# Kernel optimization log

Measured on AMD Instinct MI355X. Metric: run time of the kernel, lower is better.

Reference implementation:

```python
import jax, jax.numpy as jnp
import numpy as np

ALPHA = 0.2  # LeakyReLU negative slope


def setup_inputs() -> dict:
    key = jax.random.key(0)
    k0, k1, k2, k3 = jax.random.split(key, 4)
    N, H, W, T, V = 16, 32, 32, 16, 64
    h = jax.random.normal(k0, (N, H, W, T, V), jnp.float32)
    conv_w = jax.random.normal(k1, (3, 3, T, T), jnp.float32) * 0.05  # HWIO
    conv_b = jnp.zeros((T,), jnp.float32)
    a = jax.random.normal(k2, (2 * H * W, 1), jnp.float32) * 0.03  # ~xavier scale
    B = jax.random.uniform(k3, (V, V), jnp.float32)
    return {"h": h, "conv_w": conv_w, "conv_b": conv_b, "a": a, "B": B}


def reference(h, conv_w, conv_b, a, B):
    N, H, W, T, V = h.shape
    hv = jnp.transpose(h, (0, 4, 1, 2, 3))  # (N,V,H,W,T)

    # ConvMapping: 3x3 SAME conv over spatial dims with T as channels
    x = hv.reshape(N * V, H, W, T)
    y = jax.lax.conv_general_dilated(
        x, conv_w, (1, 1), 'SAME',
        dimension_numbers=('NHWC', 'HWIO', 'NHWC')) + conv_b
    Wh = y.reshape(N, V, H, W, T)

    # Attention logits. Original builds concat([Wh_i, Wh_j], dim=W) with trailing
    # layout (H, 2W, T) then row-major views it as (T, 2*H*W). We reproduce that
    # exact reinterpretation, but exploit additivity over i/j so the O(V^2)
    # pair tensor is never materialized.
    HW2 = 2 * H * W
    zeros = jnp.zeros_like(Wh)
    Cl = jnp.concatenate([Wh, zeros], axis=3).reshape(N, V, T, HW2)
    Cr = jnp.concatenate([zeros, Wh], axis=3).reshape(N, V, T, HW2)
    av = a[:, 0]
    Ei = jnp.einsum('bvtk,k->bvt', Cl, av)
    Ej = jnp.einsum('bvtk,k->bvt', Cr, av)
    e = jax.nn.leaky_relu(Ei[:, :, None, :] + Ej[:, None, :, :], ALPHA)  # (N,V,V,T)
    att = jax.nn.softmax(e, axis=-1)  # softmax over time dim, as in original

    # Symmetric-normalized adjacency: D^-1/2 (B + I, min-max scaled) D^-1/2
    adj = B + jnp.eye(V, dtype=B.dtype)
    adj = (adj - adj.min()) / (adj.max() - adj.min())
    d12 = 1.0 / jnp.sqrt(jnp.sum(adj, axis=1))
    adj_norm = adj * d12[:, None] * d12[None, :]

    # Aggregation: h_prime[b,p,t,i] = sum_j Wh[b,j,p,t] * att[b,i,j,t]
    # (replaces the original V^2 python loop + diag_embed matmuls)
    Whf = Wh.reshape(N, V, H * W, T)
    hp = jnp.einsum('bjpt,bijt->bpti', Whf, att)  # (N,HW,T,V)
    out = jnp.einsum('bpti,iv->bptv', hp, adj_norm)
    return jax.nn.elu(out.reshape(N, H, W, T, V))
```

## Files before the change

### kernel.cpp

```cpp
#include <hip/hip_runtime.h>
#include <hip/hip_bf16.h>
#include <math.h>

#define ALPHA_ 0.2f
#define N_ 16
#define H_ 32
#define W_ 32
#define T_ 16
#define V_ 64
#define P_ (H_*W_)

typedef __bf16 bf16x8 __attribute__((ext_vector_type(8)));
typedef float  f32x4  __attribute__((ext_vector_type(4)));

static __device__ inline bf16x8 zero8() {
    bf16x8 z;
    #pragma unroll
    for (int i = 0; i < 8; ++i) z[i] = (__bf16)0.f;
    return z;
}

static __device__ inline unsigned short bf16bits(float f) {
    __hip_bfloat16 b = __float2bfloat16(f);
    return *reinterpret_cast<unsigned short*>(&b);
}

__global__ __launch_bounds__(256) void tr_prep_k(const float* __restrict__ X,
                                                 __hip_bfloat16* __restrict__ Xt,
                                                 const float* __restrict__ CW,
                                                 const float* __restrict__ Bm,
                                                 __hip_bfloat16* __restrict__ Bfrag,
                                                 float* __restrict__ adjn) {
    int bid = blockIdx.x;
    int tid = threadIdx.x;

    if (bid == N_*34) {
        __shared__ float sd[64];
        float row[64];
        int lane = tid;
        if (tid < 64) {
            int t = lane & 15, kg = lane >> 4;
            #pragma unroll
            for (int dw = 0; dw < 3; ++dw) {
                #pragma unroll
                for (int pr = 0; pr < 2; ++pr) {
                    __hip_bfloat16* dst = Bfrag + ((size_t)((dw*2+pr)*64 + lane))*8;
                    #pragma unroll
                    for (int i = 0; i < 8; ++i) {
                        int ti = (kg & 1)*8 + i;
                        float val;
                        if (pr == 0) { int dh = kg >> 1; val = CW[((dh*3+dw)*16+ti)*16 + t]; }
                        else          val = (kg < 2) ? CW[((2*3+dw)*16+ti)*16 + t] : 0.f;
                        dst[i] = __float2bfloat16(val);
                    }
                }
            }
            int i = lane;
            float mn = 1e30f, mx = -1e30f;
            #pragma unroll
            for (int v = 0; v < 64; ++v) {
                float x = Bm[i*64 + v] + (v == i ? 1.f : 0.f);
                row[v] = x;
                mn = fminf(mn, x);
                mx = fmaxf(mx, x);
            }
            #pragma unroll
            for (int off = 32; off > 0; off >>= 1) {
                mn = fminf(mn, __shfl_xor(mn, off));
                mx = fmaxf(mx, __shfl_xor(mx, off));
            }
            float inv = 1.f / (mx - mn);
            float rs = 0.f;
            #pragma unroll
            for (int v = 0; v < 64; ++v) {
                row[v] = (row[v] - mn) * inv;
                rs += row[v];
            }
            sd[i] = rsqrtf(rs);
        }
        __syncthreads();
        if (tid < 64) {
            float d = sd[tid];
            #pragma unroll
            for (int v = 0; v < 64; ++v) adjn[tid*64 + v] = row[v] * d * sd[v];
        }
        return;
    }

    int b  = bid / 34;
    int hp = bid % 34;
    __hip_bfloat16* dstRow = Xt + ((size_t)b*34 + hp) * (size_t)(W_*V_*T_);

    if (hp == 0 || hp == 33) {
        uint4 z = {0u,0u,0u,0u};
        uint4* d = (uint4*)dstRow;
        for (int i = tid; i < (W_*V_*T_*2)/16; i += 256) d[i] = z;
        return;
    }
    int h = hp - 1;
    __shared__ float sl[4][64][17];
    const float* Xr = X + ((size_t)b*H_ + h) * (size_t)(W_*T_*V_);
    int ti = tid >> 4, v4 = (tid & 15) * 4;
    int vv = tid >> 2, tq = tid & 3;

    for (int wb = 0; wb < 8; ++wb) {
        #pragma unroll
        for (int w = 0; w < 4; ++w) {
            f32x4 x = *(const f32x4*)(Xr + (size_t)(wb*4 + w)*(T_*V_) + tid*4);
            sl[w][v4+0][ti] = x[0];
            sl[w][v4+1][ti] = x[1];
            sl[w][v4+2][ti] = x[2];
            sl[w][v4+3][ti] = x[3];
        }
        __syncthreads();
        #pragma unroll
        for (int w = 0; w < 4; ++w) {
            unsigned short u0 = bf16bits(sl[w][vv][tq*4+0]);
            unsigned short u1 = bf16bits(sl[w][vv][tq*4+1]);
            unsigned short u2 = bf16bits(sl[w][vv][tq*4+2]);
            unsigned short u3 = bf16bits(sl[w][vv][tq*4+3]);
            uint2 pk;
            pk.x = (unsigned)u0 | ((unsigned)u1 << 16);
            pk.y = (unsigned)u2 | ((unsigned)u3 << 16);
            *(uint2*)(dstRow + ((size_t)(wb*4 + w)*V_ + vv)*T_ + tq*4) = pk;
        }
        __syncthreads();
    }
}

__global__ __launch_bounds__(256) void conv_k(const __hip_bfloat16* __restrict__ Xt,
                                              const __hip_bfloat16* __restrict__ Bfrag,
                                              const float* __restrict__ CB,
                                              const float* __restrict__ av,
                                              __hip_bfloat16* __restrict__ Whb,
                                              float* __restrict__ Eihi,
                                              float* __restrict__ Eihj) {
    int orig = blockIdx.x;
    int bi   = (orig & 7) * 256 + (orig >> 3);
    int b    = bi >> 7;
    int rem  = bi & 127;
    int h    = rem >> 2;
    int vg   = rem & 3, vb = vg * 16;

    int tid = threadIdx.x, lane = tid & 63, wc = tid >> 6;
    int lm = lane & 15, kg = lane >> 4;

    bf16x8 Bf01[3], Bf2[3];
    #pragma unroll
    for (int dw = 0; dw < 3; ++dw) {
        Bf01[dw] = *(const bf16x8*)(Bfrag + (size_t)((dw*2+0)*64 + lane)*8);
        Bf2 [dw] = *(const bf16x8*)(Bfrag + (size_t)((dw*2+1)*64 + lane)*8);
    }
    float cb = CB[lm];
    f32x4 acc[8];
    #pragma unroll
    for (int wi = 0; wi < 8; ++wi) acc[wi] = (f32x4){cb, cb, cb, cb};

    const __hip_bfloat16* base01 =
        Xt + ((size_t)((b*34 + h + (kg>>1))*W_)*V_ + vb + lm)*T_ + (kg&1)*8;
    const __hip_bfloat16* base2  =
        Xt + ((size_t)((b*34 + h + 2)*W_)*V_ + vb + lm)*T_ + (kg&1)*8;

    #pragma unroll
    for (int u = 0; u < 10; ++u) {
        int wxu = wc*8 + u - 1;
        bf16x8 f01 = zero8(), f2 = zero8();
        if ((unsigned)wxu < (unsigned)W_) {
            f01 = *(const bf16x8*)(base01 + (size_t)wxu*(V_*T_));
            f2  = *(const bf16x8*)(base2  + (size_t)wxu*(V_*T_));
        }
        #pragma unroll
        for (int dw = 0; dw < 3; ++dw) {
            int wi = u - dw;
            if (wi >= 0 && wi < 8) {
                acc[wi] = __builtin_amdgcn_mfma_f32_16x16x32_bf16(f01, Bf01[dw], acc[wi], 0, 0, 0);
                acc[wi] = __builtin_amdgcn_mfma_f32_16x16x32_bf16(f2,  Bf2 [dw], acc[wi], 0, 0, 0);
            }
        }
    }

    float si[4] = {0.f,0.f,0.f,0.f}, sj[4] = {0.f,0.f,0.f,0.f};
    {
        const float* avb = av + (h & 1)*1024 + wc*8*16 + lm;
        #pragma unroll
        for (int wi = 0; wi < 8; ++wi) {
            float ai = avb[wi*16];
            float aj = avb[wi*16 + 512];
            #pragma unroll
            for (int r = 0; r < 4; ++r) {
                si[r] += acc[wi][r] * ai;
                sj[r] += acc[wi][r] * aj;
            }
        }
        #pragma unroll
        for (int off = 1; off < 16; off <<= 1) {
            #pragma unroll
            for (int r = 0; r < 4; ++r) {
                si[r] += __shfl_xor(si[r], off);
                sj[r] += __shfl_xor(sj[r], off);
            }
        }
    }
    __shared__ float sEi[4][16], sEj[4][16];
    if (lm == 0) {
        #pragma unroll
        for (int r = 0; r < 4; ++r) {
            sEi[wc][kg*4 + r] = si[r];
            sEj[wc][kg*4 + r] = sj[r];
        }
    }

    #pragma unroll
    for (int wi = 0; wi < 8; ++wi) {
        int p = h*W_ + wc*8 + wi;
        unsigned short u0 = bf16bits(acc[wi][0]);
        unsigned short u1 = bf16bits(acc[wi][1]);
        unsigned short u2 = bf16bits(acc[wi][2]);
        unsigned short u3 = bf16bits(acc[wi][3]);
        uint2 pk;
        pk.x = (unsigned)u0 | ((unsigned)u1 << 16);
        pk.y = (unsigned)u2 | ((unsigned)u3 << 16);
        *(uint2*)(Whb + ((size_t)(b*T_ + lm)*P_ + p)*V_ + vb + kg*4) = pk;
    }

    __syncthreads();
    if (tid < 16) {
        float a = sEi[0][tid] + sEi[1][tid] + sEi[2][tid] + sEi[3][tid];
        float c = sEj[0][tid] + sEj[1][tid] + sEj[2][tid] + sEj[3][tid];
        Eihi[((size_t)b*H_ + h)*V_ + vb + tid] = a;
        Eihj[((size_t)b*H_ + h)*V_ + vb + tid] = c;
    }
}

__global__ __launch_bounds__(256) void att_m_k(const float* __restrict__ Eihi,
                                               const float* __restrict__ Eihj,
                                               const float* __restrict__ adjn,
                                               __hip_bfloat16* __restrict__ Mt) {
    int b = blockIdx.x >> 6;
    int j = blockIdx.x & 63;
    int tid = threadIdx.x;
    __shared__ float s_att[64][16];

    if (tid < 64) {
        int i = tid;
        const float* ebi = Eihi + (size_t)b*H_*V_;
        const float* ebj = Eihj + (size_t)b*H_*V_;
        float ev[16];
        float mx = -1e30f;
        #pragma unroll
        for (int t = 0; t < 16; ++t) {
            float x = ebi[(2*t)*V_ + i] + ebi[(2*t+1)*V_ + i]
                    + ebj[(2*t)*V_ + j] + ebj[(2*t+1)*V_ + j];
            x = (x >= 0.f) ? x : ALPHA_ * x;
            ev[t] = x;
            mx = fmaxf(mx, x);
        }
        float s = 0.f;
        #pragma unroll
        for (int t = 0; t < 16; ++t) {
            ev[t] = __expf(ev[t] - mx);
            s += ev[t];
        }
        float invs = 1.f / s;
        #pragma unroll
        for (int t = 0; t < 16; ++t) s_att[i][t] = ev[t] * invs;
    }
    __syncthreads();

    int v = tid & 63, tq = tid >> 6;
    float acc[4] = {0.f, 0.f, 0.f, 0.f};
    for (int i = 0; i < 64; ++i) {
        float an = adjn[i*64 + v];
        #pragma unroll
        for (int u = 0; u < 4; ++u) acc[u] += s_att[i][tq*4 + u] * an;
    }
    #pragma unroll
    for (int u = 0; u < 4; ++u) {
        int t = tq*4 + u;
        Mt[(((size_t)b*T_ + t)*V_ + v)*V_ + j] = __float2bfloat16(acc[u]);
    }
}

__global__ __launch_bounds__(256) void out_k(const __hip_bfloat16* __restrict__ Whb,
                                             const __hip_bfloat16* __restrict__ Mt,
                                             float* __restrict__ out) {
    int bi = blockIdx.x;
    int pc = bi & 7;
    int t  = (bi >> 3) & 15;
    int b  = bi >> 7;

    int tid  = threadIdx.x;
    int lane = tid & 63;
    int wid  = tid >> 6;
    int lm   = lane & 15;
    int lk   = lane >> 4;

    const __hip_bfloat16* Ab = Whb + ((size_t)(b*T_ + t)*P_ + pc*128) * V_;
    const __hip_bfloat16* Bb = Mt  + (size_t)(b*T_ + t) * (V_*V_);

    f32x4 acc[2][4];
    #pragma unroll
    for (int pt = 0; pt < 2; ++pt)
        #pragma unroll
        for (int vt = 0; vt < 4; ++vt) acc[pt][vt] = (f32x4){0.f,0.f,0.f,0.f};

    #pragma unroll
    for (int kf = 0; kf < 2; ++kf) {
        int ko = kf*32 + lk*8;
        bf16x8 a0 = *(const bf16x8*)(Ab + ((size_t)((wid*2+0)*16 + lm))*V_ + ko);
        bf16x8 a1 = *(const bf16x8*)(Ab + ((size_t)((wid*2+1)*16 + lm))*V_ + ko);
        #pragma unroll
        for (int vt = 0; vt < 4; ++vt) {
            bf16x8 bf = *(const bf16x8*)(Bb + ((size_t)(vt*16 + lm))*V_ + ko);
            acc[0][vt] = __builtin_amdgcn_mfma_f32_16x16x32_bf16(a0, bf, acc[0][vt], 0, 0, 0);
            acc[1][vt] = __builtin_amdgcn_mfma_f32_16x16x32_bf16(a1, bf, acc[1][vt], 0, 0, 0);
        }
    }

    #pragma unroll
    for (int pt = 0; pt < 2; ++pt) {
        #pragma unroll
        for (int vt = 0; vt < 4; ++vt) {
            #pragma unroll
            for (int r = 0; r < 4; ++r) {
                int p  = pc*128 + (wid*2 + pt)*16 + lk*4 + r;
                int vv = vt*16 + lm;
                float x = acc[pt][vt][r];
                x = (x > 0.f) ? x : (__expf(x) - 1.f);
                out[((size_t)(b*P_ + p)*T_ + t)*V_ + vv] = x;
            }
        }
    }
}

extern "C" void kernel_launch(void* const* d_in, const int* in_sizes, int n_in,
                              void* d_out, int out_size, void* d_ws, size_t ws_size,
                              hipStream_t stream) {
    const float* X  = (const float*)d_in[0];
    const float* CW = (const float*)d_in[1];
    const float* CB = (const float*)d_in[2];
    const float* av = (const float*)d_in[3];
    const float* Bm = (const float*)d_in[4];
    float* outp = (float*)d_out;

    __hip_bfloat16* Whb = (__hip_bfloat16*)d_ws;
    __hip_bfloat16* Mt  = Whb + (size_t)N_*T_*P_*V_;
    float* Eihi = (float*)(Mt + (size_t)N_*T_*V_*V_);
    float* Eihj = Eihi + (size_t)N_*H_*V_;
    float* adjn = Eihj + (size_t)N_*H_*V_;
    __hip_bfloat16* Bfrag = (__hip_bfloat16*)(adjn + V_*V_);

    __hip_bfloat16* Xt = (__hip_bfloat16*)d_out;

    tr_prep_k<<<N_*34 + 1, 256, 0, stream>>>(X, Xt, CW, Bm, Bfrag, adjn);
    conv_k   <<<2048,      256, 0, stream>>>(Xt, Bfrag, CB, av, Whb, Eihi, Eihj);
    att_m_k  <<<N_*V_,     256, 0, stream>>>(Eihi, Eihj, adjn, Mt);
    out_k    <<<N_*T_*8,   256, 0, stream>>>(Whb, Mt, outp);
}
```

Baseline: 77.99 us.

## Fuse transpose/bf16 prep into conv via shared-memory staging; recompute adjacency in att kernel

Removes the separate transpose/prep kernel. The conv kernel now loads the fp32 input directly, converts it to bf16 and stages its three-row halo into shared memory, and builds the weight fragments from the conv weights itself. The adjacency normalization is recomputed inside each attention block, with the degree scaling folded into the softmax and output. This saves one launch and a full write and read of the transposed input. In exchange, each conv block re-reads overlapping input rows (about 3x read amplification) and every attention block redoes the small 64x64 normalization.

Result: slower. 82.51 us (+5.8%).

```diff
diff --git a/kernel.cpp b/kernel.cpp
--- a/kernel.cpp
+++ b/kernel.cpp
@@ -25,116 +25,21 @@
     return *reinterpret_cast<unsigned short*>(&b);
 }
 
-__global__ __launch_bounds__(256) void tr_prep_k(const float* __restrict__ X,
-                                                 __hip_bfloat16* __restrict__ Xt,
-                                                 const float* __restrict__ CW,
-                                                 const float* __restrict__ Bm,
-                                                 __hip_bfloat16* __restrict__ Bfrag,
-                                                 float* __restrict__ adjn) {
-    int bid = blockIdx.x;
-    int tid = threadIdx.x;
-
-    if (bid == N_*34) {
-        __shared__ float sd[64];
-        float row[64];
-        int lane = tid;
-        if (tid < 64) {
-            int t = lane & 15, kg = lane >> 4;
-            #pragma unroll
-            for (int dw = 0; dw < 3; ++dw) {
-                #pragma unroll
-                for (int pr = 0; pr < 2; ++pr) {
-                    __hip_bfloat16* dst = Bfrag + ((size_t)((dw*2+pr)*64 + lane))*8;
-                    #pragma unroll
-                    for (int i = 0; i < 8; ++i) {
-                        int ti = (kg & 1)*8 + i;
-                        float val;
-                        if (pr == 0) { int dh = kg >> 1; val = CW[((dh*3+dw)*16+ti)*16 + t]; }
-                        else          val = (kg < 2) ? CW[((2*3+dw)*16+ti)*16 + t] : 0.f;
-                        dst[i] = __float2bfloat16(val);
-                    }
-                }
-            }
-            int i = lane;
-            float mn = 1e30f, mx = -1e30f;
-            #pragma unroll
-            for (int v = 0; v < 64; ++v) {
-                float x = Bm[i*64 + v] + (v == i ? 1.f : 0.f);
-                row[v] = x;
-                mn = fminf(mn, x);
-                mx = fmaxf(mx, x);
-            }
-            #pragma unroll
-            for (int off = 32; off > 0; off >>= 1) {
-                mn = fminf(mn, __shfl_xor(mn, off));
-                mx = fmaxf(mx, __shfl_xor(mx, off));
-            }
-            float inv = 1.f / (mx - mn);
-            float rs = 0.f;
-            #pragma unroll
-            for (int v = 0; v < 64; ++v) {
-                row[v] = (row[v] - mn) * inv;
-                rs += row[v];
-            }
-            sd[i] = rsqrtf(rs);
-        }
-        __syncthreads();
-        if (tid < 64) {
-            float d = sd[tid];
-            #pragma unroll
-            for (int v = 0; v < 64; ++v) adjn[tid*64 + v] = row[v] * d * sd[v];
-        }
-        return;
-    }
-
-    int b  = bid / 34;
-    int hp = bid % 34;
-    __hip_bfloat16* dstRow = Xt + ((size_t)b*34 + hp) * (size_t)(W_*V_*T_);
-
-    if (hp == 0 || hp == 33) {
-        uint4 z = {0u,0u,0u,0u};
-        uint4* d = (uint4*)dstRow;
-        for (int i = tid; i < (W_*V_*T_*2)/16; i += 256) d[i] = z;
-        return;
-    }
-    int h = hp - 1;
-    __shared__ float sl[4][64][17];
-    const float* Xr = X + ((size_t)b*H_ + h) * (size_t)(W_*T_*V_);
-    int ti = tid >> 4, v4 = (tid & 15) * 4;
-    int vv = tid >> 2, tq = tid & 3;
-
-    for (int wb = 0; wb < 8; ++wb) {
-        #pragma unroll
-        for (int w = 0; w < 4; ++w) {
-            f32x4 x = *(const f32x4*)(Xr + (size_t)(wb*4 + w)*(T_*V_) + tid*4);
-            sl[w][v4+0][ti] = x[0];
-            sl[w][v4+1][ti] = x[1];
-            sl[w][v4+2][ti] = x[2];
-            sl[w][v4+3][ti] = x[3];
-        }
-        __syncthreads();
-        #pragma unroll
-        for (int w = 0; w < 4; ++w) {
-            unsigned short u0 = bf16bits(sl[w][vv][tq*4+0]);
-            unsigned short u1 = bf16bits(sl[w][vv][tq*4+1]);
-            unsigned short u2 = bf16bits(sl[w][vv][tq*4+2]);
-            unsigned short u3 = bf16bits(sl[w][vv][tq*4+3]);
-            uint2 pk;
-            pk.x = (unsigned)u0 | ((unsigned)u1 << 16);
-            pk.y = (unsigned)u2 | ((unsigned)u3 << 16);
-            *(uint2*)(dstRow + ((size_t)(wb*4 + w)*V_ + vv)*T_ + tq*4) = pk;
-        }
-        __syncthreads();
-    }
-}
-
-__global__ __launch_bounds__(256) void conv_k(const __hip_bfloat16* __restrict__ Xt,
-                                              const __hip_bfloat16* __restrict__ Bfrag,
+static __device__ inline __bf16 tobf(float f) {
+    unsigned short u = bf16bits(f);
+    return *reinterpret_cast<__bf16*>(&u);
+}
+
+__global__ __launch_bounds__(256) void conv_k(const float* __restrict__ X,
+                                              const float* __restrict__ CW,
                                               const float* __restrict__ CB,
                                               const float* __restrict__ av,
                                               __hip_bfloat16* __restrict__ Whb,
                                               float* __restrict__ Eihi,
                                               float* __restrict__ Eihj) {
+    __shared__ __align__(16) __hip_bfloat16 sx[3*32*2*16*8];
+    __shared__ float sEi[4][16], sEj[4][16];
+
     int orig = blockIdx.x;
     int bi   = (orig & 7) * 256 + (orig >> 3);
     int b    = bi >> 7;
@@ -148,26 +53,53 @@
     bf16x8 Bf01[3], Bf2[3];
     #pragma unroll
     for (int dw = 0; dw < 3; ++dw) {
-        Bf01[dw] = *(const bf16x8*)(Bfrag + (size_t)((dw*2+0)*64 + lane)*8);
-        Bf2 [dw] = *(const bf16x8*)(Bfrag + (size_t)((dw*2+1)*64 + lane)*8);
+        #pragma unroll
+        for (int i = 0; i < 8; ++i) {
+            int ti = (kg & 1)*8 + i;
+            int dh = kg >> 1;
+            Bf01[dw][i] = tobf(CW[((dh*3+dw)*16+ti)*16 + lm]);
+            Bf2 [dw][i] = (kg < 2) ? tobf(CW[((6+dw)*16+ti)*16 + lm]) : (__bf16)0.f;
+        }
     }
     float cb = CB[lm];
     f32x4 acc[8];
     #pragma unroll
     for (int wi = 0; wi < 8; ++wi) acc[wi] = (f32x4){cb, cb, cb, cb};
 
-    const __hip_bfloat16* base01 =
-        Xt + ((size_t)((b*34 + h + (kg>>1))*W_)*V_ + vb + lm)*T_ + (kg&1)*8;
-    const __hip_bfloat16* base2  =
-        Xt + ((size_t)((b*34 + h + 2)*W_)*V_ + vb + lm)*T_ + (kg&1)*8;
+    unsigned* sxw = (unsigned*)sx;
+    int v4i = tid & 3, tiP = (tid >> 2) & 7, sub = tid >> 5;
+    const float* Xbase = X + (size_t)b*(H_*W_*T_*V_) + (size_t)(2*tiP)*V_ + vb + v4i*4;
+    #pragma unroll
+    for (int it = 0; it < 12; ++it) {
+        int rest = it*8 + sub;
+        int w = rest & 31, r = rest >> 5;
+        int hy = h - 1 + r;
+        f32x4 xa = {0.f,0.f,0.f,0.f}, xb = {0.f,0.f,0.f,0.f};
+        if ((unsigned)hy < (unsigned)H_) {
+            const float* p = Xbase + ((size_t)hy*W_ + w)*(T_*V_);
+            xa = *(const f32x4*)(p);
+            xb = *(const f32x4*)(p + V_);
+        }
+        int widx = ((r*32 + w)*2 + (tiP>>2))*64 + v4i*16 + (tiP & 3);
+        #pragma unroll
+        for (int k2 = 0; k2 < 4; ++k2) {
+            unsigned pk = (unsigned)bf16bits(xa[k2]) | ((unsigned)bf16bits(xb[k2]) << 16);
+            sxw[widx + k2*4] = pk;
+        }
+    }
+    __syncthreads();
+
+    const char* sxb = (const char*)sx;
+    int off01 = (kg>>1)*16384 + (kg&1)*256 + lm*16;
+    int off2  = 2*16384       + (kg&1)*256 + lm*16;
 
     #pragma unroll
     for (int u = 0; u < 10; ++u) {
         int wxu = wc*8 + u - 1;
         bf16x8 f01 = zero8(), f2 = zero8();
         if ((unsigned)wxu < (unsigned)W_) {
-            f01 = *(const bf16x8*)(base01 + (size_t)wxu*(V_*T_));
-            f2  = *(const bf16x8*)(base2  + (size_t)wxu*(V_*T_));
+            f01 = *(const bf16x8*)(sxb + off01 + wxu*512);
+            f2  = *(const bf16x8*)(sxb + off2  + wxu*512);
         }
         #pragma unroll
         for (int dw = 0; dw < 3; ++dw) {
@@ -201,7 +133,6 @@
             }
         }
     }
-    __shared__ float sEi[4][16], sEj[4][16];
     if (lm == 0) {
         #pragma unroll
         for (int r = 0; r < 4; ++r) {
@@ -234,34 +165,60 @@
 
 __global__ __launch_bounds__(256) void att_m_k(const float* __restrict__ Eihi,
                                                const float* __restrict__ Eihj,
-                                               const float* __restrict__ adjn,
+                                               const float* __restrict__ Bm,
                                                __hip_bfloat16* __restrict__ Mt) {
     int b = blockIdx.x >> 6;
     int j = blockIdx.x & 63;
     int tid = threadIdx.x;
-    __shared__ float s_att[64][16];
+    __shared__ float sadj[64][65];
+    __shared__ float s_att[64][17];
+    __shared__ float sd[64];
 
     if (tid < 64) {
         int i = tid;
+        for (int r = 0; r < 64; ++r) sadj[r][i] = Bm[r*64 + i];
+        float mn = 1e30f, mx = -1e30f;
+        #pragma unroll
+        for (int v = 0; v < 64; ++v) {
+            float x = sadj[i][v] + (v == i ? 1.f : 0.f);
+            mn = fminf(mn, x);
+            mx = fmaxf(mx, x);
+        }
+        #pragma unroll
+        for (int off = 32; off > 0; off >>= 1) {
+            mn = fminf(mn, __shfl_xor(mn, off));
+            mx = fmaxf(mx, __shfl_xor(mx, off));
+        }
+        float inv = 1.f / (mx - mn);
+        float rs = 0.f;
+        #pragma unroll
+        for (int v = 0; v < 64; ++v) {
+            float x = (sadj[i][v] + (v == i ? 1.f : 0.f) - mn) * inv;
+            rs += x;
+            sadj[i][v] = x;
+        }
+        float d = rsqrtf(rs);
+        sd[i] = d;
+
         const float* ebi = Eihi + (size_t)b*H_*V_;
         const float* ebj = Eihj + (size_t)b*H_*V_;
         float ev[16];
-        float mx = -1e30f;
+        float mxe = -1e30f;
         #pragma unroll
         for (int t = 0; t < 16; ++t) {
             float x = ebi[(2*t)*V_ + i] + ebi[(2*t+1)*V_ + i]
                     + ebj[(2*t)*V_ + j] + ebj[(2*t+1)*V_ + j];
             x = (x >= 0.f) ? x : ALPHA_ * x;
             ev[t] = x;
-            mx = fmaxf(mx, x);
+            mxe = fmaxf(mxe, x);
         }
         float s = 0.f;
         #pragma unroll
         for (int t = 0; t < 16; ++t) {
-            ev[t] = __expf(ev[t] - mx);
+            ev[t] = __expf(ev[t] - mxe);
             s += ev[t];
         }
-        float invs = 1.f / s;
+        float invs = d / s;
         #pragma unroll
         for (int t = 0; t < 16; ++t) s_att[i][t] = ev[t] * invs;
     }
@@ -270,14 +227,15 @@
     int v = tid & 63, tq = tid >> 6;
     float acc[4] = {0.f, 0.f, 0.f, 0.f};
     for (int i = 0; i < 64; ++i) {
-        float an = adjn[i*64 + v];
+        float an = sadj[i][v];
         #pragma unroll
         for (int u = 0; u < 4; ++u) acc[u] += s_att[i][tq*4 + u] * an;
     }
+    float dv = sd[v];
     #pragma unroll
     for (int u = 0; u < 4; ++u) {
         int t = tq*4 + u;
-        Mt[(((size_t)b*T_ + t)*V_ + v)*V_ + j] = __float2bfloat16(acc[u]);
+        Mt[(((size_t)b*T_ + t)*V_ + v)*V_ + j] = __float2bfloat16(acc[u] * dv);
     }
 }
 
@@ -347,13 +305,8 @@
     __hip_bfloat16* Mt  = Whb + (size_t)N_*T_*P_*V_;
     float* Eihi = (float*)(Mt + (size_t)N_*T_*V_*V_);
     float* Eihj = Eihi + (size_t)N_*H_*V_;
-    float* adjn = Eihj + (size_t)N_*H_*V_;
-    __hip_bfloat16* Bfrag = (__hip_bfloat16*)(adjn + V_*V_);
-
-    __hip_bfloat16* Xt = (__hip_bfloat16*)d_out;
-
-    tr_prep_k<<<N_*34 + 1, 256, 0, stream>>>(X, Xt, CW, Bm, Bfrag, adjn);
-    conv_k   <<<2048,      256, 0, stream>>>(Xt, Bfrag, CB, av, Whb, Eihi, Eihj);
-    att_m_k  <<<N_*V_,     256, 0, stream>>>(Eihi, Eihj, adjn, Mt);
-    out_k    <<<N_*T_*8,   256, 0, stream>>>(Whb, Mt, outp);
-}
+
+    conv_k <<<2048,    256, 0, stream>>>(X, CW, CB, av, Whb, Eihi, Eihj);
+    att_m_k<<<N_*V_,   256, 0, stream>>>(Eihi, Eihj, Bm, Mt);
+    out_k  <<<N_*T_*8, 256, 0, stream>>>(Whb, Mt, outp);
+}
```
